# Optimization experiments

Hardware: AMD Instinct MI355X
Metric: run time of the kernel (lower is better)

Reference implementation:

```python
import jax, jax.numpy as jnp
import numpy as np

N = 50000      # nodes
E = 800000     # edges (avg degree 16)
F_IN = 128
H = 128        # hidden_channels
C = 10         # num_classes
S = 5          # Chebyshev order K
B = 8          # graphs in batch


def setup_inputs() -> dict:
    key = jax.random.key(0)
    ks = jax.random.split(key, 9)
    x = jax.random.normal(ks[0], (N, F_IN), jnp.float32)
    edge_index = jax.random.randint(ks[1], (2, E), 0, N, dtype=jnp.int64)
    batch = jnp.sort(jax.random.randint(ks[2], (N,), 0, B, dtype=jnp.int64))
    lambda_max = 2.0 * jnp.ones((B,), jnp.float32)
    W1 = jax.random.normal(ks[3], (S, F_IN, H), jnp.float32) * 0.05
    b1 = jax.random.normal(ks[4], (H,), jnp.float32) * 0.05
    W2 = jax.random.normal(ks[5], (S, H, H), jnp.float32) * 0.05
    b2 = jax.random.normal(ks[6], (H,), jnp.float32) * 0.05
    Wlin = jax.random.normal(ks[7], (H, C), jnp.float32) * 0.05
    blin = jax.random.normal(ks[8], (C,), jnp.float32) * 0.05
    return {"x": x, "edge_index": edge_index, "batch": batch,
            "lambda_max": lambda_max, "W1": W1, "b1": b1,
            "W2": W2, "b2": b2, "Wlin": Wlin, "blin": blin}


def _cheb_conv(x, row, col, w_edge, diag, W, b):
    # scaled Laplacian matvec: L_hat v = scatter(w_edge * v[col] -> row) + diag * v
    def Lhat(v):
        msg = v[col] * w_edge[:, None]                       # [E, d]
        return jax.ops.segment_sum(msg, row, num_segments=N) + diag[:, None] * v

    Tx0 = x
    out = Tx0 @ W[0]
    Tx1 = Lhat(Tx0)
    out = out + Tx1 @ W[1]
    for k in range(2, W.shape[0]):                           # Chebyshev recurrence
        Tx2 = 2.0 * Lhat(Tx1) - Tx0
        out = out + Tx2 @ W[k]
        Tx0, Tx1 = Tx1, Tx2
    return out + b


def reference(x, edge_index, batch, lambda_max, W1, b1, W2, b2, Wlin, blin):
    row, col = edge_index[0], edge_index[1]
    # sym-normalized Laplacian L = I - D^{-1/2} A D^{-1/2}; L_hat = 2L/lambda_max - I
    deg = jax.ops.segment_sum(jnp.ones((E,), x.dtype), row, num_segments=N)
    dis = jnp.where(deg > 0, jax.lax.rsqrt(jnp.maximum(deg, 1e-12)), 0.0)
    lam_e = lambda_max[batch[row]]                           # per-edge lambda_max
    w_edge = -2.0 * dis[row] * dis[col] / lam_e              # off-diagonal of L_hat
    diag = 2.0 / lambda_max[batch] - 1.0                     # diagonal of L_hat per node

    h = jax.nn.relu(_cheb_conv(x, row, col, w_edge, diag, W1, b1))
    h = jax.nn.relu(_cheb_conv(h, row, col, w_edge, diag, W2, b2))

    # global_mean_pool over batch assignment
    sums = jax.ops.segment_sum(h, batch, num_segments=B)     # [B, H]
    counts = jax.ops.segment_sum(jnp.ones((N, 1), h.dtype), batch, num_segments=B)
    pooled = sums / jnp.maximum(counts, 1.0)
    return pooled @ Wlin + blin                              # [B, C] logits (softmax unused in forward)
```

## Files before the change

### kernel.cpp

```cpp
#include <hip/hip_runtime.h>
#include <stdint.h>

typedef __attribute__((ext_vector_type(8))) short bf16x8;
typedef __attribute__((ext_vector_type(4))) float f32x4;

__device__ __forceinline__ float bf16lo_to_f(uint32_t u) { return __uint_as_float(u << 16); }
__device__ __forceinline__ float bf16hi_to_f(uint32_t u) { return __uint_as_float(u & 0xffff0000u); }
__device__ __forceinline__ uint16_t f_to_bf16(float f) {
    uint32_t u = __float_as_uint(f);
    uint32_t r = u + 0x7fff + ((u >> 16) & 1);
    return (uint16_t)(r >> 16);
}


#define BINCH 4096

__global__ void __launch_bounds__(256) k_bhist(const int* __restrict__ row,
                                               int* __restrict__ bhist, int E) {
    __shared__ int sh[256];
    int t = threadIdx.x;
    sh[t] = 0;
    __syncthreads();
    int stride = gridDim.x * blockDim.x;
    for (int e = blockIdx.x * blockDim.x + t; e < E; e += stride)
        atomicAdd(&sh[row[e] >> 8], 1);
    __syncthreads();
    if (sh[t]) atomicAdd(&bhist[t], sh[t]);
}

__global__ void k_bscan(const int* __restrict__ bhist, int* __restrict__ gbase,
                        int* __restrict__ gcur, int nbk) {
    __shared__ int sh[256];
    int t = threadIdx.x;
    int v = t < nbk ? bhist[t] : 0;
    sh[t] = v;
    __syncthreads();
    for (int o = 1; o < 256; o <<= 1) {
        int u = (t >= o) ? sh[t - o] : 0;
        __syncthreads();
        sh[t] += u;
        __syncthreads();
    }
    gbase[t] = sh[t] - v;
    gcur[t] = sh[t] - v;
    if (t == 255) gbase[256] = sh[255];
}

__global__ void __launch_bounds__(256) k_bin(const int* __restrict__ row,
        const int* __restrict__ col, int* __restrict__ gcur,
        uint32_t* __restrict__ bout, int E) {
    __shared__ uint32_t stage[BINCH];
    __shared__ int hist[256], hscan[256], hcur[256], gofs[256];
    int t = threadIdx.x;
    int e0 = blockIdx.x * BINCH;
    int ecnt = min(BINCH, E - e0);
    hist[t] = 0;
    __syncthreads();
    for (int i = t; i < ecnt; i += 256)
        atomicAdd(&hist[row[e0 + i] >> 8], 1);
    __syncthreads();
    int v = hist[t];
    hscan[t] = v;
    __syncthreads();
    for (int o = 1; o < 256; o <<= 1) {
        int u = (t >= o) ? hscan[t - o] : 0;
        __syncthreads();
        hscan[t] += u;
        __syncthreads();
    }
    hcur[t] = hscan[t] - v;
    __syncthreads();
    for (int i = t; i < ecnt; i += 256) {
        int r = row[e0 + i];
        int p = atomicAdd(&hcur[r >> 8], 1);
        stage[p] = (uint32_t)(r & 255) | ((uint32_t)col[e0 + i] << 8);
    }
    __syncthreads();
    if (v > 0) gofs[t] = atomicAdd(&gcur[t], v);
    __syncthreads();
    for (int i = t; i < ecnt; i += 256) {
        int lo = 0, hi = 255;
        while (lo < hi) { int mid = (lo + hi) >> 1; if (hscan[mid] > i) hi = mid; else lo = mid + 1; }
        int b = lo;
        int local = i - (hscan[b] - hist[b]);
        bout[gofs[b] + local] = stage[i];
    }
}

__global__ void __launch_bounds__(256) k_deg2(const uint32_t* __restrict__ bout,
        const int* __restrict__ gbase, int* __restrict__ deg,
        int* __restrict__ psum, int N) {
    __shared__ int cnt[256];
    __shared__ int red[256];
    int t = threadIdx.x, b = blockIdx.x;
    cnt[t] = 0;
    __syncthreads();
    int s = gbase[b], epos = gbase[b + 1];
    for (int i = s + t; i < epos; i += 256)
        atomicAdd(&cnt[bout[i] & 255], 1);
    __syncthreads();
    int n = b * 256 + t;
    int d = cnt[t];
    if (n < N) deg[n] = d;
    red[t] = (n < N) ? ((d + 7) & ~7) : 0;
    __syncthreads();
    for (int o = 128; o > 0; o >>= 1) {
        if (t < o) red[t] += red[t + o];
        __syncthreads();
    }
    if (t == 0) psum[b] = red[0];
}

__global__ void k_offs(const int* __restrict__ deg, const int* __restrict__ psum,
                       int* __restrict__ offs,
                       const int* __restrict__ batch, const float* __restrict__ lam,
                       float* __restrict__ dis, float* __restrict__ diag,
                       int N, int nb) {
    __shared__ int pre[256];
    __shared__ int sh[256];
    int t = threadIdx.x, b = blockIdx.x;
    pre[t] = (t < b) ? psum[t] : 0;
    __syncthreads();
    for (int o = 128; o > 0; o >>= 1) {
        if (t < o) pre[t] += pre[t + o];
        __syncthreads();
    }
    int base = pre[0];
    __syncthreads();
    int idx = b * 256 + t;
    int d = idx < N ? deg[idx] : 0;
    int v = (d + 7) & ~7;
    sh[t] = v;
    __syncthreads();
    for (int o = 1; o < 256; o <<= 1) {
        int u = (t >= o) ? sh[t - o] : 0;
        __syncthreads();
        sh[t] += u;
        __syncthreads();
    }
    if (idx < N) {
        offs[idx] = base + sh[t] - v;
        dis[idx] = d > 0 ? rsqrtf((float)d) : 0.f;
        diag[idx] = 2.f / lam[batch[idx]] - 1.f;
    }
    if (b == nb - 1 && t == 255) offs[N] = base + sh[255];
}

__global__ void __launch_bounds__(256) k_ew(const uint32_t* __restrict__ bout,
        const int* __restrict__ gbase, const int* __restrict__ offs,
        const float* __restrict__ dis, const float* __restrict__ diag,
        uint2* __restrict__ ew, int N) {
    __shared__ int cur[256];
    __shared__ float srw[256];
    int t = threadIdx.x, b = blockIdx.x;
    int n = b * 256 + t;
    int o0 = n < N ? offs[n] : 0;
    cur[t] = o0;
    srw[t] = (n < N) ? (-dis[n] * (diag[n] + 1.0f)) : 0.f;
    __syncthreads();
    int s = gbase[b], epos = gbase[b + 1];
    for (int i = s + t; i < epos; i += 256) {
        uint32_t v = bout[i];
        int r = (int)(v & 255u);
        int c = (int)(v >> 8);
        int p = atomicAdd(&cur[r], 1);
        float w = srw[r] * dis[c];
        ew[p] = make_uint2((uint32_t)c << 8, __float_as_uint(w));
    }
    __syncthreads();
    if (n < N) {
        int e = cur[t];
        int pe = o0 + ((e - o0 + 7) & ~7);
        uint2 pad = make_uint2((uint32_t)N << 8, 0u);
        for (int p = e; p < pe; p++) ew[p] = pad;
    }
}

__global__ void k_prepw(const float* __restrict__ W1, uint16_t* __restrict__ Wt1,
                        const float* __restrict__ W2, uint16_t* __restrict__ Wt2) {
    int i = blockIdx.x * blockDim.x + threadIdx.x;
    const float* W = W1; uint16_t* Wt = Wt1;
    if (i >= 128 * 640) { i -= 128 * 640; W = W2; Wt = Wt2; }
    int o = i / 640, kk = i % 640;
    Wt[(size_t)o * 640 + kk] = f_to_bf16(W[(size_t)kk * 128 + o]);
}

__global__ void __launch_bounds__(256) k_castx(const float* __restrict__ x,
        uint16_t* __restrict__ Txg, int N) {
    int n = (blockIdx.x * blockDim.x + threadIdx.x) >> 6;
    int lane = threadIdx.x & 63;
    if (n > N) return;
    size_t ss32 = (size_t)(N + 1) * 64;
    if (n == N) {
#pragma unroll
        for (int s = 0; s < 5; s++)
            ((uint32_t*)Txg)[s * ss32 + (size_t)N * 64 + lane] = 0u;
        return;
    }
    float2 v = ((const float2*)x)[(size_t)n * 64 + lane];
    uint32_t p = (uint32_t)f_to_bf16(v.x) | ((uint32_t)f_to_bf16(v.y) << 16);
    ((uint32_t*)Txg)[(size_t)n * 64 + lane] = p;
}

__global__ void __launch_bounds__(256) k_lhat(uint16_t* Txg,
        const int* __restrict__ offs, const uint2* __restrict__ ew,
        const float* __restrict__ diag, int N,
        int src, int dst, int prev, float alpha, int use_prev) {
    int n = (blockIdx.x * blockDim.x + threadIdx.x) >> 6;
    int lane = threadIdx.x & 63;
    if (n >= N) return;
    int beg = offs[n], end = offs[n + 1];
    size_t sb = (size_t)(N + 1) * 256;
    const uint8_t* srcs = (const uint8_t*)Txg + (size_t)src * sb;
    uint32_t lo4 = (uint32_t)lane * 4;
    float ax = 0.f, ay = 0.f;
    for (int e = beg; e < end; e += 8) {
        const uint4* ep = (const uint4*)(ew + e);
        uint4 a = ep[0], b4 = ep[1], c4 = ep[2], d4 = ep[3];
        uint32_t co[8]; float wv[8];
        co[0] = a.x;  wv[0] = __uint_as_float(a.y);
        co[1] = a.z;  wv[1] = __uint_as_float(a.w);
        co[2] = b4.x; wv[2] = __uint_as_float(b4.y);
        co[3] = b4.z; wv[3] = __uint_as_float(b4.w);
        co[4] = c4.x; wv[4] = __uint_as_float(c4.y);
        co[5] = c4.z; wv[5] = __uint_as_float(c4.w);
        co[6] = d4.x; wv[6] = __uint_as_float(d4.y);
        co[7] = d4.z; wv[7] = __uint_as_float(d4.w);
        uint32_t q[8];
#pragma unroll
        for (int u = 0; u < 8; u++)
            q[u] = *(const uint32_t*)(srcs + (co[u] + lo4));
#pragma unroll
        for (int u = 0; u < 8; u++) {
            ax = fmaf(wv[u], bf16lo_to_f(q[u]), ax);
            ay = fmaf(wv[u], bf16hi_to_f(q[u]), ay);
        }
    }
    float dgn = diag[n];
    uint32_t roff = ((uint32_t)n << 8) + lo4;
    uint32_t qs = *(const uint32_t*)(srcs + roff);
    ax = fmaf(dgn, bf16lo_to_f(qs), ax);
    ay = fmaf(dgn, bf16hi_to_f(qs), ay);
    float fx = alpha * ax, fy = alpha * ay;
    if (use_prev) {
        const uint8_t* prs = (const uint8_t*)Txg + (size_t)prev * sb;
        uint32_t qp = *(const uint32_t*)(prs + roff);
        fx -= bf16lo_to_f(qp);
        fy -= bf16hi_to_f(qp);
    }
    uint32_t outv = (uint32_t)f_to_bf16(fx) | ((uint32_t)f_to_bf16(fy) << 16);
    *(uint32_t*)((uint8_t*)Txg + (size_t)dst * sb + roff) = outv;
}

#define BM 128
#define BK 64
#define LDT 72
#define LDC 132

__global__ void __launch_bounds__(256) k_gemm(
        const uint16_t* __restrict__ A, size_t sstride,
        const uint16_t* __restrict__ Bt,
        const float* __restrict__ bias,
        uint16_t* __restrict__ out2b,
        float* __restrict__ pooled,
        const int* __restrict__ batch,
        int M, int Kdim) {
    __shared__ uint16_t smem[BM * LDT + 128 * LDT];
    uint16_t* As = smem;
    uint16_t* Bs = smem + BM * LDT;
    uint16_t* Ct = smem;
    int t = threadIdx.x;
    int w = t >> 6, lane = t & 63;
    int row0 = blockIdx.x * BM;
    int mrow = (w >> 1) * 64, ncol = (w & 1) * 64;

    int ar[4], akc[4];
#pragma unroll
    for (int rep = 0; rep < 4; rep++) {
        int d = rep * 256 + t;
        ar[rep] = d >> 3; akc[rep] = d & 7;
    }

    f32x4 acc[4][4];
#pragma unroll
    for (int i = 0; i < 4; i++)
#pragma unroll
        for (int j = 0; j < 4; j++) acc[i][j] = (f32x4){0.f, 0.f, 0.f, 0.f};

    bf16x8 pa[4], pb[4];
#pragma unroll
    for (int rep = 0; rep < 4; rep++) {
        int grow = row0 + ar[rep];
        int kk = akc[rep] * 8;
        bf16x8 va = {0, 0, 0, 0, 0, 0, 0, 0};
        if (grow < M)
            va = *(const bf16x8*)(A + (size_t)(kk >> 7) * sstride + (size_t)grow * 128 + (kk & 127));
        pa[rep] = va;
        pb[rep] = *(const bf16x8*)(Bt + (size_t)ar[rep] * Kdim + kk);
    }

    for (int k0 = 0; k0 < Kdim; k0 += BK) {
#pragma unroll
        for (int rep = 0; rep < 4; rep++) {
            *(bf16x8*)(&As[ar[rep] * LDT + akc[rep] * 8]) = pa[rep];
            *(bf16x8*)(&Bs[ar[rep] * LDT + akc[rep] * 8]) = pb[rep];
        }
        __syncthreads();
        int kn = k0 + BK;
        if (kn < Kdim) {
#pragma unroll
            for (int rep = 0; rep < 4; rep++) {
                int grow = row0 + ar[rep];
                int kk = kn + akc[rep] * 8;
                bf16x8 va = {0, 0, 0, 0, 0, 0, 0, 0};
                if (grow < M)
                    va = *(const bf16x8*)(A + (size_t)(kk >> 7) * sstride + (size_t)grow * 128 + (kk & 127));
                pa[rep] = va;
                pb[rep] = *(const bf16x8*)(Bt + (size_t)ar[rep] * Kdim + kk);
            }
        }
#pragma unroll
        for (int ks = 0; ks < BK; ks += 32) {
            bf16x8 af[4], bfr[4];
#pragma unroll
            for (int i = 0; i < 4; i++) {
                int r = mrow + i * 16 + (lane & 15);
                af[i] = *(const bf16x8*)(&As[r * LDT + ks + (lane >> 4) * 8]);
            }
#pragma unroll
            for (int j = 0; j < 4; j++) {
                int c = ncol + j * 16 + (lane & 15);
                bfr[j] = *(const bf16x8*)(&Bs[c * LDT + ks + (lane >> 4) * 8]);
            }
#pragma unroll
            for (int i = 0; i < 4; i++)
#pragma unroll
                for (int j = 0; j < 4; j++)
                    acc[i][j] = __builtin_amdgcn_mfma_f32_16x16x32_bf16(af[i], bfr[j], acc[i][j], 0, 0, 0);
        }
        __syncthreads();
    }

#pragma unroll
    for (int j = 0; j < 4; j++) {
        int c = ncol + j * 16 + (lane & 15);
        float bv = bias[c];
#pragma unroll
        for (int i = 0; i < 4; i++) {
            int rloc = mrow + i * 16 + (lane >> 4) * 4;
#pragma unroll
            for (int r = 0; r < 4; r++) {
                float v = acc[i][j][r] + bv;
                v = v > 0.f ? v : 0.f;
                Ct[(rloc + r) * LDC + c] = f_to_bf16(v);
            }
        }
    }
    __syncthreads();

    if (out2b) {
#pragma unroll
        for (int rep = 0; rep < 8; rep++) {
            int d = rep * 256 + t;
            int r = d >> 4, c8 = (d & 15) * 8;
            int grow = row0 + r;
            if (grow < M) {
                bf16x8 v = *(const bf16x8*)(&Ct[r * LDC + c8]);
                *(bf16x8*)(out2b + (size_t)grow * 128 + c8) = v;
            }
        }
    }
    if (pooled) {
        int f = t & 127, r0 = (t >> 7) * 64;
        float accp = 0.f;
        int curb = -1;
        for (int r = r0; r < r0 + 64; ++r) {
            int grow = row0 + r;
            if (grow >= M) break;
            int b = batch[grow];
            if (b != curb) {
                if (curb >= 0) atomicAdd(&pooled[curb * 128 + f], accp);
                accp = 0.f; curb = b;
            }
            accp += __uint_as_float(((uint32_t)Ct[r * LDC + f]) << 16);
        }
        if (curb >= 0) atomicAdd(&pooled[curb * 128 + f], accp);
    }
}

__global__ void k_final(const float* __restrict__ pooled, const int* __restrict__ batch,
                        const float* __restrict__ Wlin, const float* __restrict__ blin,
                        float* __restrict__ out, int N, int B_, int C_) {
    __shared__ int cnt[64];
    int t = threadIdx.x;
    if (t < B_) {
        auto lb = [&](int v) {
            int lo = 0, hi = N;
            while (lo < hi) {
                int mid = (lo + hi) >> 1;
                if (batch[mid] < v) lo = mid + 1; else hi = mid;
            }
            return lo;
        };
        cnt[t] = lb(t + 1) - lb(t);
    }
    __syncthreads();
    if (t < B_ * C_) {
        int b = t / C_, c = t % C_;
        float inv = 1.f / fmaxf((float)cnt[b], 1.f);
        float acc = blin[c];
        for (int f = 0; f < 128; ++f) acc += pooled[b * 128 + f] * inv * Wlin[f * C_ + c];
        out[t] = acc;
    }
}

extern "C" void kernel_launch(void* const* d_in, const int* in_sizes, int n_in,
                              void* d_out, int out_size, void* d_ws, size_t ws_size,
                              hipStream_t stream) {
    const float* x    = (const float*)d_in[0];
    const int*   edge = (const int*)d_in[1];
    const int*   batch= (const int*)d_in[2];
    const float* lam  = (const float*)d_in[3];
    const float* W1   = (const float*)d_in[4];
    const float* b1   = (const float*)d_in[5];
    const float* W2   = (const float*)d_in[6];
    const float* b2   = (const float*)d_in[7];
    const float* Wlin = (const float*)d_in[8];
    const float* blin = (const float*)d_in[9];
    const int E  = in_sizes[1] / 2;
    const int N  = in_sizes[2];
    const int B_ = in_sizes[3];
    const int* row = edge;
    const int* col = edge + E;

    char* ws = (char*)d_ws;
    size_t off = 0;
    auto take = [&](size_t bytes) -> char* {
        char* p = ws + off;
        off = (off + bytes + 255) & ~(size_t)255;
        return p;
    };
    uint16_t* Txg    = (uint16_t*)take((size_t)5 * (N + 1) * 128 * 2);
    uint2*    ew     = (uint2*)take(((size_t)E + 8 * (size_t)N) * 8);
    uint32_t* bout   = (uint32_t*)take((size_t)E * 4);
    int*      deg    = (int*)take((size_t)N * 4);
    int*      offs   = (int*)take((size_t)(N + 1) * 4);
    float*    dis    = (float*)take((size_t)N * 4);
    float*    diag   = (float*)take((size_t)N * 4);
    uint16_t* Wt1    = (uint16_t*)take((size_t)128 * 640 * 2);
    uint16_t* Wt2    = (uint16_t*)take((size_t)128 * 640 * 2);
    float*    pooled = (float*)take((size_t)B_ * 128 * 4);
    int*      bhist  = (int*)take(257 * 4);
    int*      gbase  = (int*)take(257 * 4);
    int*      gcur   = (int*)take(257 * 4);
    const int nb = (N + 255) / 256;
    int*      psum   = (int*)take((size_t)nb * 4);

    hipMemsetAsync(pooled, 0, (size_t)B_ * 128 * 4 + 257 * 4, stream);

    k_bhist<<<112, 256, 0, stream>>>(row, bhist, E);
    k_bscan<<<1, 256, 0, stream>>>(bhist, gbase, gcur, nb);
    k_bin<<<(E + BINCH - 1) / BINCH, 256, 0, stream>>>(row, col, gcur, bout, E);
    k_deg2<<<nb, 256, 0, stream>>>(bout, gbase, deg, psum, N);
    k_offs<<<nb, 256, 0, stream>>>(deg, psum, offs, batch, lam, dis, diag, N, nb);
    k_ew<<<nb, 256, 0, stream>>>(bout, gbase, offs, dis, diag, ew, N);
    k_prepw<<<(2 * 128 * 640) / 256, 256, 0, stream>>>(W1, Wt1, W2, Wt2);
    k_castx<<<(N + 4) / 4, 256, 0, stream>>>(x, Txg, N);

    const int lblocks = (N + 3) / 4;
    const int gblocks = (N + BM - 1) / BM;
    const size_t ss = (size_t)(N + 1) * 128;

    k_lhat<<<lblocks, 256, 0, stream>>>(Txg, offs, ew, diag, N, 0, 1, 0, 1.f, 0);
    k_lhat<<<lblocks, 256, 0, stream>>>(Txg, offs, ew, diag, N, 1, 2, 0, 2.f, 1);
    k_lhat<<<lblocks, 256, 0, stream>>>(Txg, offs, ew, diag, N, 2, 3, 1, 2.f, 1);
    k_lhat<<<lblocks, 256, 0, stream>>>(Txg, offs, ew, diag, N, 3, 4, 2, 2.f, 1);
    k_gemm<<<gblocks, 256, 0, stream>>>(Txg, ss, Wt1, b1,
                                        Txg , (float*)nullptr, batch, N, 640);

    k_lhat<<<lblocks, 256, 0, stream>>>(Txg, offs, ew, diag, N, 0, 1, 0, 1.f, 0);
    k_lhat<<<lblocks, 256, 0, stream>>>(Txg, offs, ew, diag, N, 1, 2, 0, 2.f, 1);
    k_lhat<<<lblocks, 256, 0, stream>>>(Txg, offs, ew, diag, N, 2, 3, 1, 2.f, 1);
    k_lhat<<<lblocks, 256, 0, stream>>>(Txg, offs, ew, diag, N, 3, 4, 2, 2.f, 1);
    k_gemm<<<gblocks, 256, 0, stream>>>(Txg, ss, Wt2, b2,
                                        (uint16_t*)nullptr, pooled, batch, N, 640);

    k_final<<<1, 128, 0, stream>>>(pooled, batch, Wlin, blin, (float*)d_out, N, B_, 10);
}
```

Baseline: 474.5 us.

## Gather int8 per-row-scaled features in Laplacian SpMM, keep bf16 copy for GEMM

Each Chebyshev basis vector is now also stored as int8 with a per-node absmax scale, and the sparse Laplacian gather reads these int8 rows (128 bytes per neighbor) instead of bf16 rows. A bf16 copy is still written for the GEMM. The lhat kernel splits each wave into two half-waves that handle alternating edges, prefetches the next edge batch, and reduces with a shuffle. The goal is to halve gather bandwidth, which dominates the SpMM. The cost is extra quantization error that compounds through the recurrence, plus extra writes and a max-reduction per node.

```diff
diff --git a/kernel.cpp b/kernel.cpp
--- a/kernel.cpp
+++ b/kernel.cpp
@@ -29,7 +29,7 @@
 }
 
 __global__ void k_bscan(const int* __restrict__ bhist, int* __restrict__ gbase,
-                        int* __restrict__ gcur, int nbk) {
+                        int* __restrict__ gcur, float* __restrict__ mS, int nbk, int N) {
     __shared__ int sh[256];
     int t = threadIdx.x;
     int v = t < nbk ? bhist[t] : 0;
@@ -44,6 +44,7 @@
     gbase[t] = sh[t] - v;
     gcur[t] = sh[t] - v;
     if (t == 255) gbase[256] = sh[255];
+    if (t < 5) mS[(size_t)t * (N + 1) + N] = 0.f;
 }
 
 __global__ void __launch_bounds__(256) k_bin(const int* __restrict__ row,
@@ -165,13 +166,13 @@
         int c = (int)(v >> 8);
         int p = atomicAdd(&cur[r], 1);
         float w = srw[r] * dis[c];
-        ew[p] = make_uint2((uint32_t)c << 8, __float_as_uint(w));
+        ew[p] = make_uint2((uint32_t)c << 7, __float_as_uint(w));
     }
     __syncthreads();
     if (n < N) {
         int e = cur[t];
         int pe = o0 + ((e - o0 + 7) & ~7);
-        uint2 pad = make_uint2((uint32_t)N << 8, 0u);
+        uint2 pad = make_uint2((uint32_t)N << 7, 0u);
         for (int p = e; p < pe; p++) ew[p] = pad;
     }
 }
@@ -186,23 +187,25 @@
 }
 
 __global__ void __launch_bounds__(256) k_castx(const float* __restrict__ x,
-        uint16_t* __restrict__ Txg, int N) {
+        uint16_t* __restrict__ Txb, int8_t* __restrict__ Txq,
+        float* __restrict__ mS, int N) {
     int n = (blockIdx.x * blockDim.x + threadIdx.x) >> 6;
     int lane = threadIdx.x & 63;
-    if (n > N) return;
-    size_t ss32 = (size_t)(N + 1) * 64;
-    if (n == N) {
-#pragma unroll
-        for (int s = 0; s < 5; s++)
-            ((uint32_t*)Txg)[s * ss32 + (size_t)N * 64 + lane] = 0u;
-        return;
-    }
+    if (n >= N) return;
     float2 v = ((const float2*)x)[(size_t)n * 64 + lane];
     uint32_t p = (uint32_t)f_to_bf16(v.x) | ((uint32_t)f_to_bf16(v.y) << 16);
-    ((uint32_t*)Txg)[(size_t)n * 64 + lane] = p;
-}
-
-__global__ void __launch_bounds__(256) k_lhat(uint16_t* Txg,
+    ((uint32_t*)Txb)[(size_t)n * 64 + lane] = p;
+    float m = fmaxf(fabsf(v.x), fabsf(v.y));
+    for (int o = 1; o < 64; o <<= 1) m = fmaxf(m, __shfl_xor(m, o));
+    float inv = m > 0.f ? 127.f / m : 0.f;
+    int qx = (int)rintf(v.x * inv), qy = (int)rintf(v.y * inv);
+    *(uint16_t*)(Txq + (size_t)n * 128 + 2 * lane) = (uint16_t)((qx & 0xff) | ((qy & 0xff) << 8));
+    if (lane == 0) mS[n] = m > 0.f ? m * (1.f / 127.f) : 0.f;
+}
+
+__global__ void __launch_bounds__(256) k_lhat(
+        int8_t* __restrict__ Txq, uint16_t* __restrict__ Txb,
+        float* __restrict__ mS,
         const int* __restrict__ offs, const uint2* __restrict__ ew,
         const float* __restrict__ diag, int N,
         int src, int dst, int prev, float alpha, int use_prev) {
@@ -210,46 +213,86 @@
     int lane = threadIdx.x & 63;
     if (n >= N) return;
     int beg = offs[n], end = offs[n + 1];
-    size_t sb = (size_t)(N + 1) * 256;
-    const uint8_t* srcs = (const uint8_t*)Txg + (size_t)src * sb;
-    uint32_t lo4 = (uint32_t)lane * 4;
-    float ax = 0.f, ay = 0.f;
-    for (int e = beg; e < end; e += 8) {
-        const uint4* ep = (const uint4*)(ew + e);
-        uint4 a = ep[0], b4 = ep[1], c4 = ep[2], d4 = ep[3];
-        uint32_t co[8]; float wv[8];
-        co[0] = a.x;  wv[0] = __uint_as_float(a.y);
-        co[1] = a.z;  wv[1] = __uint_as_float(a.w);
-        co[2] = b4.x; wv[2] = __uint_as_float(b4.y);
-        co[3] = b4.z; wv[3] = __uint_as_float(b4.w);
-        co[4] = c4.x; wv[4] = __uint_as_float(c4.y);
-        co[5] = c4.z; wv[5] = __uint_as_float(c4.w);
-        co[6] = d4.x; wv[6] = __uint_as_float(d4.y);
-        co[7] = d4.z; wv[7] = __uint_as_float(d4.w);
-        uint32_t q[8];
-#pragma unroll
-        for (int u = 0; u < 8; u++)
-            q[u] = *(const uint32_t*)(srcs + (co[u] + lo4));
-#pragma unroll
-        for (int u = 0; u < 8; u++) {
-            ax = fmaf(wv[u], bf16lo_to_f(q[u]), ax);
-            ay = fmaf(wv[u], bf16hi_to_f(q[u]), ay);
-        }
-    }
-    float dgn = diag[n];
-    uint32_t roff = ((uint32_t)n << 8) + lo4;
-    uint32_t qs = *(const uint32_t*)(srcs + roff);
-    ax = fmaf(dgn, bf16lo_to_f(qs), ax);
-    ay = fmaf(dgn, bf16hi_to_f(qs), ay);
-    float fx = alpha * ax, fy = alpha * ay;
+    int h = lane >> 5, g = lane & 31;
+    size_t sq = (size_t)(N + 1) * 128;
+    const int8_t* srcq = Txq + (size_t)src * sq;
+    const float* msrc = mS + (size_t)src * (N + 1);
+    uint32_t lo4 = (uint32_t)g * 4;
+    const uint2* ewh = ew + h;
+    float a0 = 0.f, a1 = 0.f, a2 = 0.f, a3 = 0.f;
+    if (beg < end) {
+        uint2 ep[4];
+#pragma unroll
+        for (int p = 0; p < 4; p++) ep[p] = ewh[beg + 2 * p];
+        int e = beg;
+        while (true) {
+            uint32_t q[4]; float mm[4], wv[4];
+#pragma unroll
+            for (int p = 0; p < 4; p++) {
+                uint32_t co = ep[p].x;
+                wv[p] = __uint_as_float(ep[p].y);
+                q[p] = *(const uint32_t*)(srcq + co + lo4);
+                mm[p] = *(const float*)((const char*)msrc + (co >> 5));
+            }
+            int e2 = e + 8;
+            bool more = e2 < end;
+            uint2 epn[4];
+            if (more) {
+#pragma unroll
+                for (int p = 0; p < 4; p++) epn[p] = ewh[e2 + 2 * p];
+            }
+#pragma unroll
+            for (int p = 0; p < 4; p++) {
+                float f = wv[p] * mm[p];
+                a0 = fmaf(f, (float)(int)(int8_t)(q[p] & 0xff), a0);
+                a1 = fmaf(f, (float)(int)(int8_t)((q[p] >> 8) & 0xff), a1);
+                a2 = fmaf(f, (float)(int)(int8_t)((q[p] >> 16) & 0xff), a2);
+                a3 = fmaf(f, (float)(int)(int8_t)(q[p] >> 24), a3);
+            }
+            if (!more) break;
+            e = e2;
+#pragma unroll
+            for (int p = 0; p < 4; p++) ep[p] = epn[p];
+        }
+    }
+    a0 += __shfl_xor(a0, 32);
+    a1 += __shfl_xor(a1, 32);
+    a2 += __shfl_xor(a2, 32);
+    a3 += __shfl_xor(a3, 32);
+    uint32_t rq = (uint32_t)n * 128 + lo4;
+    uint32_t qs = *(const uint32_t*)(srcq + rq);
+    float ssc = msrc[n] * diag[n];
+    a0 = fmaf(ssc, (float)(int)(int8_t)(qs & 0xff), a0);
+    a1 = fmaf(ssc, (float)(int)(int8_t)((qs >> 8) & 0xff), a1);
+    a2 = fmaf(ssc, (float)(int)(int8_t)((qs >> 16) & 0xff), a2);
+    a3 = fmaf(ssc, (float)(int)(int8_t)(qs >> 24), a3);
+    float f0 = alpha * a0, f1 = alpha * a1, f2 = alpha * a2, f3 = alpha * a3;
     if (use_prev) {
-        const uint8_t* prs = (const uint8_t*)Txg + (size_t)prev * sb;
-        uint32_t qp = *(const uint32_t*)(prs + roff);
-        fx -= bf16lo_to_f(qp);
-        fy -= bf16hi_to_f(qp);
-    }
-    uint32_t outv = (uint32_t)f_to_bf16(fx) | ((uint32_t)f_to_bf16(fy) << 16);
-    *(uint32_t*)((uint8_t*)Txg + (size_t)dst * sb + roff) = outv;
+        uint32_t qp = *(const uint32_t*)(Txq + (size_t)prev * sq + rq);
+        float sp = mS[(size_t)prev * (N + 1) + n];
+        f0 = fmaf(-sp, (float)(int)(int8_t)(qp & 0xff), f0);
+        f1 = fmaf(-sp, (float)(int)(int8_t)((qp >> 8) & 0xff), f1);
+        f2 = fmaf(-sp, (float)(int)(int8_t)((qp >> 16) & 0xff), f2);
+        f3 = fmaf(-sp, (float)(int)(int8_t)(qp >> 24), f3);
+    }
+    if (h == 0) {
+        uint2 pk;
+        pk.x = (uint32_t)f_to_bf16(f0) | ((uint32_t)f_to_bf16(f1) << 16);
+        pk.y = (uint32_t)f_to_bf16(f2) | ((uint32_t)f_to_bf16(f3) << 16);
+        *(uint2*)(Txb + (size_t)dst * (size_t)(N + 1) * 128 + (size_t)n * 128 + g * 4) = pk;
+    }
+    float m = fmaxf(fmaxf(fabsf(f0), fabsf(f1)), fmaxf(fabsf(f2), fabsf(f3)));
+#pragma unroll
+    for (int o = 1; o < 32; o <<= 1) m = fmaxf(m, __shfl_xor(m, o));
+    float inv = m > 0.f ? 127.f / m : 0.f;
+    if (h == 0) {
+        int q0 = (int)rintf(f0 * inv), q1 = (int)rintf(f1 * inv);
+        int q2 = (int)rintf(f2 * inv), q3 = (int)rintf(f3 * inv);
+        uint32_t pkq = (uint32_t)(q0 & 0xff) | ((uint32_t)(q1 & 0xff) << 8) |
+                       ((uint32_t)(q2 & 0xff) << 16) | ((uint32_t)(q3 & 0xff) << 24);
+        *(uint32_t*)(Txq + (size_t)dst * sq + rq) = pkq;
+    }
+    if (lane == 0) mS[(size_t)dst * (N + 1) + n] = m * (1.f / 127.f);
 }
 
 #define BM 128
@@ -262,6 +305,8 @@
         const uint16_t* __restrict__ Bt,
         const float* __restrict__ bias,
         uint16_t* __restrict__ out2b,
+        int8_t* __restrict__ out2q,
+        float* __restrict__ msOut,
         float* __restrict__ pooled,
         const int* __restrict__ batch,
         int M, int Kdim) {
@@ -368,6 +413,31 @@
                 bf16x8 v = *(const bf16x8*)(&Ct[r * LDC + c8]);
                 *(bf16x8*)(out2b + (size_t)grow * 128 + c8) = v;
             }
+        }
+    }
+    if (out2q) {
+        int r = t >> 1, half = t & 1;
+        int grow = row0 + r;
+        float vmax = 0.f;
+        for (int j = 0; j < 32; j++) {
+            uint32_t u = *(const uint32_t*)(&Ct[r * LDC + half * 64 + j * 2]);
+            vmax = fmaxf(vmax, fmaxf(fabsf(bf16lo_to_f(u)), fabsf(bf16hi_to_f(u))));
+        }
+        vmax = fmaxf(vmax, __shfl_xor(vmax, 1));
+        if (grow < M) {
+            float inv = vmax > 0.f ? 127.f / vmax : 0.f;
+            for (int j0 = 0; j0 < 16; j0++) {
+                uint32_t u0 = *(const uint32_t*)(&Ct[r * LDC + half * 64 + j0 * 4]);
+                uint32_t u1 = *(const uint32_t*)(&Ct[r * LDC + half * 64 + j0 * 4 + 2]);
+                int q0 = (int)rintf(bf16lo_to_f(u0) * inv);
+                int q1 = (int)rintf(bf16hi_to_f(u0) * inv);
+                int q2 = (int)rintf(bf16lo_to_f(u1) * inv);
+                int q3 = (int)rintf(bf16hi_to_f(u1) * inv);
+                uint32_t pk = (uint32_t)(q0 & 0xff) | ((uint32_t)(q1 & 0xff) << 8) |
+                              ((uint32_t)(q2 & 0xff) << 16) | ((uint32_t)(q3 & 0xff) << 24);
+                *(uint32_t*)(out2q + (size_t)grow * 128 + half * 64 + j0 * 4) = pk;
+            }
+            if (half == 0) msOut[grow] = vmax * (1.f / 127.f);
         }
     }
     if (pooled) {
@@ -440,9 +510,10 @@
         off = (off + bytes + 255) & ~(size_t)255;
         return p;
     };
-    uint16_t* Txg    = (uint16_t*)take((size_t)5 * (N + 1) * 128 * 2);
+    uint16_t* Txb    = (uint16_t*)take((size_t)5 * (N + 1) * 128 * 2);
+    int8_t*   Txq    = (int8_t*)take((size_t)5 * (N + 1) * 128);
     uint2*    ew     = (uint2*)take(((size_t)E + 8 * (size_t)N) * 8);
-    uint32_t* bout   = (uint32_t*)take((size_t)E * 4);
+    float*    mS     = (float*)take((size_t)5 * (N + 1) * 4);
     int*      deg    = (int*)take((size_t)N * 4);
     int*      offs   = (int*)take((size_t)(N + 1) * 4);
     float*    dis    = (float*)take((size_t)N * 4);
@@ -455,35 +526,38 @@
     int*      gcur   = (int*)take(257 * 4);
     const int nb = (N + 255) / 256;
     int*      psum   = (int*)take((size_t)nb * 4);
+    uint32_t* bout   = (uint32_t*)((char*)Txb + (size_t)4 * (N + 1) * 256);
 
     hipMemsetAsync(pooled, 0, (size_t)B_ * 128 * 4 + 257 * 4, stream);
 
     k_bhist<<<112, 256, 0, stream>>>(row, bhist, E);
-    k_bscan<<<1, 256, 0, stream>>>(bhist, gbase, gcur, nb);
+    k_bscan<<<1, 256, 0, stream>>>(bhist, gbase, gcur, mS, nb, N);
     k_bin<<<(E + BINCH - 1) / BINCH, 256, 0, stream>>>(row, col, gcur, bout, E);
     k_deg2<<<nb, 256, 0, stream>>>(bout, gbase, deg, psum, N);
     k_offs<<<nb, 256, 0, stream>>>(deg, psum, offs, batch, lam, dis, diag, N, nb);
     k_ew<<<nb, 256, 0, stream>>>(bout, gbase, offs, dis, diag, ew, N);
     k_prepw<<<(2 * 128 * 640) / 256, 256, 0, stream>>>(W1, Wt1, W2, Wt2);
-    k_castx<<<(N + 4) / 4, 256, 0, stream>>>(x, Txg, N);
+    k_castx<<<(N + 3) / 4, 256, 0, stream>>>(x, Txb, Txq, mS, N);
 
     const int lblocks = (N + 3) / 4;
     const int gblocks = (N + BM - 1) / BM;
     const size_t ss = (size_t)(N + 1) * 128;
 
-    k_lhat<<<lblocks, 256, 0, stream>>>(Txg, offs, ew, diag, N, 0, 1, 0, 1.f, 0);
-    k_lhat<<<lblocks, 256, 0, stream>>>(Txg, offs, ew, diag, N, 1, 2, 0, 2.f, 1);
-    k_lhat<<<lblocks, 256, 0, stream>>>(Txg, offs, ew, diag, N, 2, 3, 1, 2.f, 1);
-    k_lhat<<<lblocks, 256, 0, stream>>>(Txg, offs, ew, diag, N, 3, 4, 2, 2.f, 1);
-    k_gemm<<<gblocks, 256, 0, stream>>>(Txg, ss, Wt1, b1,
-                                        Txg , (float*)nullptr, batch, N, 640);
-
-    k_lhat<<<lblocks, 256, 0, stream>>>(Txg, offs, ew, diag, N, 0, 1, 0, 1.f, 0);
-    k_lhat<<<lblocks, 256, 0, stream>>>(Txg, offs, ew, diag, N, 1, 2, 0, 2.f, 1);
-    k_lhat<<<lblocks, 256, 0, stream>>>(Txg, offs, ew, diag, N, 2, 3, 1, 2.f, 1);
-    k_lhat<<<lblocks, 256, 0, stream>>>(Txg, offs, ew, diag, N, 3, 4, 2, 2.f, 1);
-    k_gemm<<<gblocks, 256, 0, stream>>>(Txg, ss, Wt2, b2,
-                                        (uint16_t*)nullptr, pooled, batch, N, 640);
+    k_lhat<<<lblocks, 256, 0, stream>>>(Txq, Txb, mS, offs, ew, diag, N, 0, 1, 0, 1.f, 0);
+    k_lhat<<<lblocks, 256, 0, stream>>>(Txq, Txb, mS, offs, ew, diag, N, 1, 2, 0, 2.f, 1);
+    k_lhat<<<lblocks, 256, 0, stream>>>(Txq, Txb, mS, offs, ew, diag, N, 2, 3, 1, 2.f, 1);
+    k_lhat<<<lblocks, 256, 0, stream>>>(Txq, Txb, mS, offs, ew, diag, N, 3, 4, 2, 2.f, 1);
+    k_gemm<<<gblocks, 256, 0, stream>>>(Txb, ss, Wt1, b1,
+                                        Txb , Txq , mS ,
+                                        (float*)nullptr, batch, N, 640);
+
+    k_lhat<<<lblocks, 256, 0, stream>>>(Txq, Txb, mS, offs, ew, diag, N, 0, 1, 0, 1.f, 0);
+    k_lhat<<<lblocks, 256, 0, stream>>>(Txq, Txb, mS, offs, ew, diag, N, 1, 2, 0, 2.f, 1);
+    k_lhat<<<lblocks, 256, 0, stream>>>(Txq, Txb, mS, offs, ew, diag, N, 2, 3, 1, 2.f, 1);
+    k_lhat<<<lblocks, 256, 0, stream>>>(Txq, Txb, mS, offs, ew, diag, N, 3, 4, 2, 2.f, 1);
+    k_gemm<<<gblocks, 256, 0, stream>>>(Txb, ss, Wt2, b2,
+                                        (uint16_t*)nullptr, (int8_t*)nullptr, (float*)nullptr,
+                                        pooled, batch, N, 640);
 
     k_final<<<1, 128, 0, stream>>>(pooled, batch, Wlin, blin, (float*)d_out, N, B_, 10);
 }
```

Measured after the change: 469.3 us. About the same (-1.1%).

## Pack edge records into 32-bit and split SpMM wavefront into two half-waves

Applied to the files above, without the earlier changes.

Edge records shrink from 8-byte (col<<8, fp32 weight) to 4-byte (16-bit col index, bf16 weight). They are stored in an interleaved order so each half of a wavefront reads 4 edges per uint4 load. The L_hat kernel now has 32 lanes per half-wave, each handling 4 features with 8-byte gathers, then combines the halves with a shuffle. Edge loads are prefetched one step ahead, and a per-node uint4 header replaces separate offs/diag reads. The binned-edge scratch buffer is aliased into the last Tx slot. This lowers edge-stream bandwidth and gather instruction count, at the cost of bf16 edge weights and a 16-bit column index that only holds for N < 65536.

```diff
diff --git a/kernel.cpp b/kernel.cpp
--- a/kernel.cpp
+++ b/kernel.cpp
@@ -115,6 +115,7 @@
                        int* __restrict__ offs,
                        const int* __restrict__ batch, const float* __restrict__ lam,
                        float* __restrict__ dis, float* __restrict__ diag,
+                       uint4* __restrict__ nh,
                        int N, int nb) {
     __shared__ int pre[256];
     __shared__ int sh[256];
@@ -139,9 +140,13 @@
         __syncthreads();
     }
     if (idx < N) {
-        offs[idx] = base + sh[t] - v;
+        int beg = base + sh[t] - v;
+        float dgv = 2.f / lam[batch[idx]] - 1.f;
+        offs[idx] = beg;
         dis[idx] = d > 0 ? rsqrtf((float)d) : 0.f;
-        diag[idx] = 2.f / lam[batch[idx]] - 1.f;
+        diag[idx] = dgv;
+        nh[idx] = make_uint4((uint32_t)beg, (uint32_t)(base + sh[t] - v + v),
+                             __float_as_uint(dgv), 0u);
     }
     if (b == nb - 1 && t == 255) offs[N] = base + sh[255];
 }
@@ -149,13 +154,15 @@
 __global__ void __launch_bounds__(256) k_ew(const uint32_t* __restrict__ bout,
         const int* __restrict__ gbase, const int* __restrict__ offs,
         const float* __restrict__ dis, const float* __restrict__ diag,
-        uint2* __restrict__ ew, int N) {
+        uint32_t* __restrict__ ew, int N) {
     __shared__ int cur[256];
+    __shared__ int bs0[256];
     __shared__ float srw[256];
     int t = threadIdx.x, b = blockIdx.x;
     int n = b * 256 + t;
     int o0 = n < N ? offs[n] : 0;
-    cur[t] = o0;
+    cur[t] = 0;
+    bs0[t] = o0;
     srw[t] = (n < N) ? (-dis[n] * (diag[n] + 1.0f)) : 0.f;
     __syncthreads();
     int s = gbase[b], epos = gbase[b + 1];
@@ -163,16 +170,19 @@
         uint32_t v = bout[i];
         int r = (int)(v & 255u);
         int c = (int)(v >> 8);
-        int p = atomicAdd(&cur[r], 1);
+        int idx = atomicAdd(&cur[r], 1);
         float w = srw[r] * dis[c];
-        ew[p] = make_uint2((uint32_t)c << 8, __float_as_uint(w));
+        int pos = bs0[r] + (idx & ~7) + ((idx & 1) << 2) + ((idx >> 1) & 3);
+        ew[pos] = (uint32_t)c | ((uint32_t)f_to_bf16(w) << 16);
     }
     __syncthreads();
     if (n < N) {
-        int e = cur[t];
-        int pe = o0 + ((e - o0 + 7) & ~7);
-        uint2 pad = make_uint2((uint32_t)N << 8, 0u);
-        for (int p = e; p < pe; p++) ew[p] = pad;
+        int cnt = cur[t];
+        int pe = (cnt + 7) & ~7;
+        for (int i = cnt; i < pe; i++) {
+            int pos = o0 + (i & ~7) + ((i & 1) << 2) + ((i >> 1) & 3);
+            ew[pos] = (uint32_t)N;
+        }
     }
 }
 
@@ -186,7 +196,7 @@
 }
 
 __global__ void __launch_bounds__(256) k_castx(const float* __restrict__ x,
-        uint16_t* __restrict__ Txg, int N) {
+        uint16_t* __restrict__ Txb, int N) {
     int n = (blockIdx.x * blockDim.x + threadIdx.x) >> 6;
     int lane = threadIdx.x & 63;
     if (n > N) return;
@@ -194,62 +204,78 @@
     if (n == N) {
 #pragma unroll
         for (int s = 0; s < 5; s++)
-            ((uint32_t*)Txg)[s * ss32 + (size_t)N * 64 + lane] = 0u;
+            ((uint32_t*)Txb)[s * ss32 + (size_t)N * 64 + lane] = 0u;
         return;
     }
     float2 v = ((const float2*)x)[(size_t)n * 64 + lane];
     uint32_t p = (uint32_t)f_to_bf16(v.x) | ((uint32_t)f_to_bf16(v.y) << 16);
-    ((uint32_t*)Txg)[(size_t)n * 64 + lane] = p;
-}
-
-__global__ void __launch_bounds__(256) k_lhat(uint16_t* Txg,
-        const int* __restrict__ offs, const uint2* __restrict__ ew,
-        const float* __restrict__ diag, int N,
+    ((uint32_t*)Txb)[(size_t)n * 64 + lane] = p;
+}
+
+__global__ void __launch_bounds__(256) k_lhat(uint16_t* __restrict__ Txb,
+        const uint4* __restrict__ nh, const uint32_t* __restrict__ ew,
+        int N,
         int src, int dst, int prev, float alpha, int use_prev) {
     int n = (blockIdx.x * blockDim.x + threadIdx.x) >> 6;
     int lane = threadIdx.x & 63;
     if (n >= N) return;
-    int beg = offs[n], end = offs[n + 1];
+    int h = lane >> 5, g = lane & 31;
     size_t sb = (size_t)(N + 1) * 256;
-    const uint8_t* srcs = (const uint8_t*)Txg + (size_t)src * sb;
-    uint32_t lo4 = (uint32_t)lane * 4;
-    float ax = 0.f, ay = 0.f;
-    for (int e = beg; e < end; e += 8) {
-        const uint4* ep = (const uint4*)(ew + e);
-        uint4 a = ep[0], b4 = ep[1], c4 = ep[2], d4 = ep[3];
-        uint32_t co[8]; float wv[8];
-        co[0] = a.x;  wv[0] = __uint_as_float(a.y);
-        co[1] = a.z;  wv[1] = __uint_as_float(a.w);
-        co[2] = b4.x; wv[2] = __uint_as_float(b4.y);
-        co[3] = b4.z; wv[3] = __uint_as_float(b4.w);
-        co[4] = c4.x; wv[4] = __uint_as_float(c4.y);
-        co[5] = c4.z; wv[5] = __uint_as_float(c4.w);
-        co[6] = d4.x; wv[6] = __uint_as_float(d4.y);
-        co[7] = d4.z; wv[7] = __uint_as_float(d4.w);
-        uint32_t q[8];
-#pragma unroll
-        for (int u = 0; u < 8; u++)
-            q[u] = *(const uint32_t*)(srcs + (co[u] + lo4));
-#pragma unroll
-        for (int u = 0; u < 8; u++) {
-            ax = fmaf(wv[u], bf16lo_to_f(q[u]), ax);
-            ay = fmaf(wv[u], bf16hi_to_f(q[u]), ay);
-        }
-    }
-    float dgn = diag[n];
-    uint32_t roff = ((uint32_t)n << 8) + lo4;
-    uint32_t qs = *(const uint32_t*)(srcs + roff);
-    ax = fmaf(dgn, bf16lo_to_f(qs), ax);
-    ay = fmaf(dgn, bf16hi_to_f(qs), ay);
-    float fx = alpha * ax, fy = alpha * ay;
-    if (use_prev) {
-        const uint8_t* prs = (const uint8_t*)Txg + (size_t)prev * sb;
-        uint32_t qp = *(const uint32_t*)(prs + roff);
-        fx -= bf16lo_to_f(qp);
-        fy -= bf16hi_to_f(qp);
-    }
-    uint32_t outv = (uint32_t)f_to_bf16(fx) | ((uint32_t)f_to_bf16(fy) << 16);
-    *(uint32_t*)((uint8_t*)Txg + (size_t)dst * sb + roff) = outv;
+    const uint8_t* srcs = (const uint8_t*)Txb + (size_t)src * sb;
+    uint32_t g8 = (uint32_t)g * 8;
+    uint4 hh = nh[n];
+    int e = (int)hh.x, end = (int)hh.y;
+    float dgn = __uint_as_float(hh.z);
+    float a0 = 0.f, a1 = 0.f, a2 = 0.f, a3 = 0.f;
+    if (e < end) {
+        const uint4* ep = (const uint4*)(ew + e + h * 4);
+        int npk = (end - e) >> 3;
+        uint4 c = ep[0];
+        int pk = 0;
+        while (true) {
+            bool more = (pk + 1) < npk;
+            uint4 cn;
+            if (more) cn = ep[(pk + 1) * 2];
+#pragma unroll
+            for (int u = 0; u < 4; u++) {
+                uint32_t cw = (&c.x)[u];
+                uint32_t addr = (cw & 0xffffu) << 8;
+                float w = __uint_as_float(cw & 0xffff0000u);
+                uint2 q = *(const uint2*)(srcs + addr + g8);
+                a0 = fmaf(w, bf16lo_to_f(q.x), a0);
+                a1 = fmaf(w, bf16hi_to_f(q.x), a1);
+                a2 = fmaf(w, bf16lo_to_f(q.y), a2);
+                a3 = fmaf(w, bf16hi_to_f(q.y), a3);
+            }
+            if (!more) break;
+            c = cn;
+            pk++;
+        }
+    }
+    a0 += __shfl_xor(a0, 32);
+    a1 += __shfl_xor(a1, 32);
+    a2 += __shfl_xor(a2, 32);
+    a3 += __shfl_xor(a3, 32);
+    if (h == 0) {
+        size_t ro = (size_t)n * 256 + g8;
+        uint2 qs = *(const uint2*)(srcs + ro);
+        a0 = fmaf(dgn, bf16lo_to_f(qs.x), a0);
+        a1 = fmaf(dgn, bf16hi_to_f(qs.x), a1);
+        a2 = fmaf(dgn, bf16lo_to_f(qs.y), a2);
+        a3 = fmaf(dgn, bf16hi_to_f(qs.y), a3);
+        float f0 = alpha * a0, f1 = alpha * a1, f2 = alpha * a2, f3 = alpha * a3;
+        if (use_prev) {
+            uint2 qp = *(const uint2*)((const uint8_t*)Txb + (size_t)prev * sb + ro);
+            f0 -= bf16lo_to_f(qp.x);
+            f1 -= bf16hi_to_f(qp.x);
+            f2 -= bf16lo_to_f(qp.y);
+            f3 -= bf16hi_to_f(qp.y);
+        }
+        uint2 pk2;
+        pk2.x = (uint32_t)f_to_bf16(f0) | ((uint32_t)f_to_bf16(f1) << 16);
+        pk2.y = (uint32_t)f_to_bf16(f2) | ((uint32_t)f_to_bf16(f3) << 16);
+        *(uint2*)((uint8_t*)Txb + (size_t)dst * sb + ro) = pk2;
+    }
 }
 
 #define BM 128
@@ -440,13 +466,13 @@
         off = (off + bytes + 255) & ~(size_t)255;
         return p;
     };
-    uint16_t* Txg    = (uint16_t*)take((size_t)5 * (N + 1) * 128 * 2);
-    uint2*    ew     = (uint2*)take(((size_t)E + 8 * (size_t)N) * 8);
-    uint32_t* bout   = (uint32_t*)take((size_t)E * 4);
+    uint16_t* Txb    = (uint16_t*)take((size_t)5 * (N + 1) * 128 * 2);
+    uint32_t* ew     = (uint32_t*)take(((size_t)E + 8 * (size_t)N) * 4);
     int*      deg    = (int*)take((size_t)N * 4);
     int*      offs   = (int*)take((size_t)(N + 1) * 4);
     float*    dis    = (float*)take((size_t)N * 4);
     float*    diag   = (float*)take((size_t)N * 4);
+    uint4*    nh     = (uint4*)take((size_t)N * 16);
     uint16_t* Wt1    = (uint16_t*)take((size_t)128 * 640 * 2);
     uint16_t* Wt2    = (uint16_t*)take((size_t)128 * 640 * 2);
     float*    pooled = (float*)take((size_t)B_ * 128 * 4);
@@ -455,34 +481,37 @@
     int*      gcur   = (int*)take(257 * 4);
     const int nb = (N + 255) / 256;
     int*      psum   = (int*)take((size_t)nb * 4);
+    uint32_t* bout   = (uint32_t*)((char*)Txb + (size_t)4 * (N + 1) * 256);
 
     hipMemsetAsync(pooled, 0, (size_t)B_ * 128 * 4 + 257 * 4, stream);
+
+    const int nchunks = (E + BINCH - 1) / BINCH;
 
     k_bhist<<<112, 256, 0, stream>>>(row, bhist, E);
     k_bscan<<<1, 256, 0, stream>>>(bhist, gbase, gcur, nb);
-    k_bin<<<(E + BINCH - 1) / BINCH, 256, 0, stream>>>(row, col, gcur, bout, E);
+    k_bin<<<nchunks, 256, 0, stream>>>(row, col, gcur, bout, E);
     k_deg2<<<nb, 256, 0, stream>>>(bout, gbase, deg, psum, N);
-    k_offs<<<nb, 256, 0, stream>>>(deg, psum, offs, batch, lam, dis, diag, N, nb);
+    k_offs<<<nb, 256, 0, stream>>>(deg, psum, offs, batch, lam, dis, diag, nh, N, nb);
     k_ew<<<nb, 256, 0, stream>>>(bout, gbase, offs, dis, diag, ew, N);
     k_prepw<<<(2 * 128 * 640) / 256, 256, 0, stream>>>(W1, Wt1, W2, Wt2);
-    k_castx<<<(N + 4) / 4, 256, 0, stream>>>(x, Txg, N);
+    k_castx<<<(N + 4) / 4, 256, 0, stream>>>(x, Txb, N);
 
     const int lblocks = (N + 3) / 4;
     const int gblocks = (N + BM - 1) / BM;
     const size_t ss = (size_t)(N + 1) * 128;
 
-    k_lhat<<<lblocks, 256, 0, stream>>>(Txg, offs, ew, diag, N, 0, 1, 0, 1.f, 0);
-    k_lhat<<<lblocks, 256, 0, stream>>>(Txg, offs, ew, diag, N, 1, 2, 0, 2.f, 1);
-    k_lhat<<<lblocks, 256, 0, stream>>>(Txg, offs, ew, diag, N, 2, 3, 1, 2.f, 1);
-    k_lhat<<<lblocks, 256, 0, stream>>>(Txg, offs, ew, diag, N, 3, 4, 2, 2.f, 1);
-    k_gemm<<<gblocks, 256, 0, stream>>>(Txg, ss, Wt1, b1,
-                                        Txg , (float*)nullptr, batch, N, 640);
-
-    k_lhat<<<lblocks, 256, 0, stream>>>(Txg, offs, ew, diag, N, 0, 1, 0, 1.f, 0);
-    k_lhat<<<lblocks, 256, 0, stream>>>(Txg, offs, ew, diag, N, 1, 2, 0, 2.f, 1);
-    k_lhat<<<lblocks, 256, 0, stream>>>(Txg, offs, ew, diag, N, 2, 3, 1, 2.f, 1);
-    k_lhat<<<lblocks, 256, 0, stream>>>(Txg, offs, ew, diag, N, 3, 4, 2, 2.f, 1);
-    k_gemm<<<gblocks, 256, 0, stream>>>(Txg, ss, Wt2, b2,
+    k_lhat<<<lblocks, 256, 0, stream>>>(Txb, nh, ew, N, 0, 1, 0, 1.f, 0);
+    k_lhat<<<lblocks, 256, 0, stream>>>(Txb, nh, ew, N, 1, 2, 0, 2.f, 1);
+    k_lhat<<<lblocks, 256, 0, stream>>>(Txb, nh, ew, N, 2, 3, 1, 2.f, 1);
+    k_lhat<<<lblocks, 256, 0, stream>>>(Txb, nh, ew, N, 3, 4, 2, 2.f, 1);
+    k_gemm<<<gblocks, 256, 0, stream>>>(Txb, ss, Wt1, b1,
+                                        Txb , (float*)nullptr, batch, N, 640);
+
+    k_lhat<<<lblocks, 256, 0, stream>>>(Txb, nh, ew, N, 0, 1, 0, 1.f, 0);
+    k_lhat<<<lblocks, 256, 0, stream>>>(Txb, nh, ew, N, 1, 2, 0, 2.f, 1);
+    k_lhat<<<lblocks, 256, 0, stream>>>(Txb, nh, ew, N, 2, 3, 1, 2.f, 1);
+    k_lhat<<<lblocks, 256, 0, stream>>>(Txb, nh, ew, N, 3, 4, 2, 2.f, 1);
+    k_gemm<<<gblocks, 256, 0, stream>>>(Txb, ss, Wt2, b2,
                                         (uint16_t*)nullptr, pooled, batch, N, 640);
 
     k_final<<<1, 128, 0, stream>>>(pooled, batch, Wlin, blin, (float*)d_out, N, B_, 10);
```

New measurement: 470.0 us. No clear change (-1.0%).
